# Performance work log

Hardware: AMD Instinct MI355X
Metric: run time of the kernel (lower is better)

## Reference

```python
import jax, jax.numpy as jnp
import numpy as np

DIM = 192
HEADS = 16
DIM_HEAD = 64
INNER = HEADS * DIM_HEAD  # 1024
B, N = 8, 1024


def setup_inputs() -> dict:
    key = jax.random.key(0)
    ks = jax.random.split(key, 8)
    x = jax.random.normal(ks[0], (B, N, DIM), dtype=jnp.float32)
    shift = jax.random.normal(ks[1], (B, 1, DIM), dtype=jnp.float32)
    scale = jax.random.normal(ks[2], (B, 1, DIM), dtype=jnp.float32)
    norm_w = jnp.ones((DIM,), dtype=jnp.float32)
    norm_b = jnp.zeros((DIM,), dtype=jnp.float32)
    w_qkv = jax.random.normal(ks[3], (DIM, 3 * INNER), dtype=jnp.float32) * (DIM ** -0.5)
    w_out = jax.random.normal(ks[4], (INNER, DIM), dtype=jnp.float32) * (INNER ** -0.5)
    b_out = jnp.zeros((DIM,), dtype=jnp.float32)
    return {"x": x, "shift": shift, "scale": scale, "norm_w": norm_w,
            "norm_b": norm_b, "w_qkv": w_qkv, "w_out": w_out, "b_out": b_out}


def _layernorm(x, w, b, eps=1e-5):
    mu = jnp.mean(x, axis=-1, keepdims=True)
    var = jnp.mean(jnp.square(x - mu), axis=-1, keepdims=True)
    return (x - mu) * jax.lax.rsqrt(var + eps) * w + b


def reference(x, shift, scale, norm_w, norm_b, w_qkv, w_out, b_out):
    h = _layernorm(x, norm_w, norm_b)
    h = h * (1.0 + scale) + shift  # adaLN modulation, broadcast over tokens
    qkv = h @ w_qkv  # [B, N, 3*INNER]
    q, k, v = jnp.split(qkv, 3, axis=-1)
    # [B, N, INNER] -> [B, H, N, Dh]
    def split_heads(t):
        return t.reshape(B, N, HEADS, DIM_HEAD).transpose(0, 2, 1, 3)
    q, k, v = split_heads(q), split_heads(k), split_heads(v)
    scores = jnp.einsum('bhnd,bhmd->bhnm', q, k) * (DIM_HEAD ** -0.5)
    attn = jax.nn.softmax(scores, axis=-1)
    out = jnp.einsum('bhnm,bhmd->bhnd', attn, v)  # [B, H, N, Dh]
    out = out.transpose(0, 2, 1, 3).reshape(B, N, INNER)
    return out @ w_out + b_out
```

## Files before the change

kernel.cpp:

```cpp
#include <hip/hip_runtime.h>

#define DIM 192
#define NB 8
#define NTOK 1024
#define HEADS 16
#define DH 64
#define INNER 1024
#define ROWS (NB * NTOK)

typedef __bf16 bf16x8 __attribute__((ext_vector_type(8)));
typedef float f32x4 __attribute__((ext_vector_type(4)));
typedef float f32x16 __attribute__((ext_vector_type(16)));
typedef unsigned int u32x4 __attribute__((ext_vector_type(4)));

__device__ inline unsigned short f2bf(float f) {
    union { float f; unsigned u; } v; v.f = f;
    unsigned r = v.u + 0x7FFF + ((v.u >> 16) & 1);
    return (unsigned short)(r >> 16);
}

__device__ inline unsigned pk2(float a, float b) {
    __bf16 x = (__bf16)a, y = (__bf16)b;
    unsigned short ux = __builtin_bit_cast(unsigned short, x);
    unsigned short uy = __builtin_bit_cast(unsigned short, y);
    return (unsigned)ux | ((unsigned)uy << 16);
}

__device__ inline void gl_lds16(const unsigned short* g, unsigned short* l) {
    __builtin_amdgcn_global_load_lds(
        (const __attribute__((address_space(1))) void*)g,
        (__attribute__((address_space(3))) void*)l, 16, 0, 0);
}

__device__ inline size_t fragIdx(int row, int k, int depth) {
    return ((size_t)(row >> 5) * ((size_t)depth * 4) +
            (size_t)(((k >> 4) * 2 + ((k >> 3) & 1)) * 32 + (row & 31))) * 8 + (k & 7);
}

__global__ __launch_bounds__(256) void k_pre(
    const float* __restrict__ x, const float* __restrict__ shift,
    const float* __restrict__ scale, const float* __restrict__ nw,
    const float* __restrict__ nb, const float* __restrict__ wqkv,
    const float* __restrict__ wout,
    unsigned short* __restrict__ hF, unsigned short* __restrict__ wF,
    unsigned short* __restrict__ woF) {
    int bid = blockIdx.x;
    if (bid < 2048) {
        int row = bid * 4 + (threadIdx.x >> 6);
        int lane = threadIdx.x & 63;
        const float* xr = x + row * DIM;
        float v0 = xr[lane], v1 = xr[lane + 64], v2 = xr[lane + 128];
        float s = v0 + v1 + v2;
        #pragma unroll
        for (int m = 1; m < 64; m <<= 1) s += __shfl_xor(s, m);
        float mean = s * (1.0f / DIM);
        float d0 = v0 - mean, d1 = v1 - mean, d2 = v2 - mean;
        float q = d0 * d0 + d1 * d1 + d2 * d2;
        #pragma unroll
        for (int m = 1; m < 64; m <<= 1) q += __shfl_xor(q, m);
        float rs = rsqrtf(q * (1.0f / DIM) + 1e-5f);
        int b = row >> 10;
        float vv[3] = {v0, v1, v2};
        #pragma unroll
        for (int i = 0; i < 3; i++) {
            int d = lane + 64 * i;
            float val = (vv[i] - mean) * rs * nw[d] + nb[d];
            val = val * (1.0f + scale[b * DIM + d]) + shift[b * DIM + d];
            hF[fragIdx(row, d, DIM)] = f2bf(val);
        }
    } else if (bid < 4352) {
        int idx = (bid - 2048) * 256 + threadIdx.x;
        int k = idx / 3072, c = idx % 3072;
        wF[fragIdx(c, k, DIM)] = f2bf(wqkv[idx]);
    } else {
        int idx = (bid - 4352) * 256 + threadIdx.x;
        int k = idx / 192, c = idx % 192;
        woF[fragIdx(c, k, INNER)] = f2bf(wout[idx]);
    }
}

__global__ __launch_bounds__(256, 3) void k_qkv(
    const unsigned short* __restrict__ hF, const unsigned short* __restrict__ wF,
    unsigned short* __restrict__ qm, unsigned short* __restrict__ km,
    unsigned short* __restrict__ vtm) {
    const float QSC = 0.125f * 1.4426950408889634f;
    int tid = threadIdx.x;
    int wave = tid >> 6, lane = tid & 63;
    int l31 = lane & 31, hi = lane >> 5;
    int c0 = blockIdx.x * 64 + (wave >> 1) * 32;
    int typ = c0 >> 10;
    int hd  = (c0 & 1023) >> 6;
    int coff = c0 & 32;

    const unsigned short* Ab = wF + (size_t)(c0 >> 5) * 768 * 8;
    bf16x8 af[12];
    #pragma unroll
    for (int kc = 0; kc < 12; kc++)
        af[kc] = *(const bf16x8*)(Ab + ((kc * 2 + hi) * 32 + l31) * 8);

    #pragma unroll
    for (int ns = 0; ns < 2; ns++) {
        int n0 = blockIdx.y * 128 + (wave & 1) * 64 + ns * 32;
        const unsigned short* Bb = hF + (size_t)(n0 >> 5) * 768 * 8;
        f32x16 acc;
        #pragma unroll
        for (int r = 0; r < 16; r++) acc[r] = 0.f;
        #pragma unroll
        for (int kc = 0; kc < 12; kc++) {
            bf16x8 bf = *(const bf16x8*)(Bb + ((kc * 2 + hi) * 32 + l31) * 8);
            acc = __builtin_amdgcn_mfma_f32_32x32x16_bf16(af[kc], bf, acc, 0, 0, 0);
        }
        int n = n0 + l31, bb = n >> 10, nm = n & 1023;
        if (typ < 2) {
            float sc = (typ == 0) ? QSC : 1.0f;
            unsigned short* base = (typ == 0 ? qm : km) +
                ((size_t)(bb * 16 + hd) * 1024 + nm) * 64;
            #pragma unroll
            for (int rg = 0; rg < 4; rg++) {
                uint2 val;
                val.x = pk2(acc[rg * 4 + 0] * sc, acc[rg * 4 + 1] * sc);
                val.y = pk2(acc[rg * 4 + 2] * sc, acc[rg * 4 + 3] * sc);
                *(uint2*)(base + coff + rg * 8 + hi * 4) = val;
            }
        } else {
            unsigned short* base = vtm + (size_t)(bb * 16 + hd) * 65536 + nm;
            #pragma unroll
            for (int r = 0; r < 16; r++) {
                int d = coff + (r & 3) + 8 * (r >> 2) + 4 * hi;
                base[(size_t)d * 1024] = f2bf(acc[r]);
            }
        }
    }
}

__global__ __launch_bounds__(512, 4) void k_attn(
    const unsigned short* __restrict__ qm, const unsigned short* __restrict__ km,
    const unsigned short* __restrict__ vtm, unsigned short* __restrict__ attnF) {
    __shared__ __align__(128) unsigned short Kb[2][4096];
    __shared__ __align__(128) unsigned short Vb[3][4096];

    int tid = threadIdx.x;
    int wave = tid >> 6, lane = tid & 63;
    int l31 = lane & 31, hi = lane >> 5;
    int bh = blockIdx.x, qt = blockIdx.y;
    int qbase = qt * 256 + wave * 32;
    const unsigned short* Q = qm + (size_t)bh * NTOK * DH;
    const unsigned short* K = km + (size_t)bh * NTOK * DH;
    const unsigned short* VT = vtm + (size_t)bh * DH * NTOK;

    bf16x8 qf[4];
    #pragma unroll
    for (int c = 0; c < 4; c++)
        qf[c] = *(const bf16x8*)(Q + (qbase + l31) * DH + c * 16 + hi * 8);

    float l_half = 0.f;
    f32x16 accO[2];
    #pragma unroll
    for (int dt = 0; dt < 2; dt++)
        #pragma unroll
        for (int r = 0; r < 16; r++) accO[dt][r] = 0.f;

    auto stageK = [&](int b, int t) {
        int off = tid * 16;
        int row = off >> 7, col = off & 127;
        int scol = col ^ ((row & 7) << 4);
        gl_lds16(K + (t * 64 + row) * DH + (scol >> 1),
                 (unsigned short*)((char*)Kb[b] + off));
    };
    auto stageV = [&](int b, int t) {
        int off = tid * 16;
        int row = off >> 7, col = off & 127;
        int scol = col ^ ((row & 7) << 4);
        gl_lds16(VT + (size_t)row * NTOK + t * 64 + (scol >> 1),
                 (unsigned short*)((char*)Vb[b] + off));
    };
    auto ldK = [&](int b, int row, int col) -> bf16x8 {
        int scol = col ^ ((row & 7) << 4);
        return *(const bf16x8*)((const char*)Kb[b] + row * 128 + scol);
    };
    auto ldV = [&](int b, int row, int col) -> bf16x8 {
        int scol = col ^ ((row & 7) << 4);
        return *(const bf16x8*)((const char*)Vb[b] + row * 128 + scol);
    };
    auto packP = [&](const f32x16& P, bf16x8& w0, bf16x8& w1) {
        u32x4 A, B;
        {
            auto r0 = __builtin_amdgcn_permlane32_swap(pk2(P[0], P[1]), pk2(P[4], P[5]), false, false);
            auto r1 = __builtin_amdgcn_permlane32_swap(pk2(P[2], P[3]), pk2(P[6], P[7]), false, false);
            A[0] = r0[0]; A[1] = r1[0]; A[2] = r0[1]; A[3] = r1[1];
        }
        {
            auto r0 = __builtin_amdgcn_permlane32_swap(pk2(P[8], P[9]), pk2(P[12], P[13]), false, false);
            auto r1 = __builtin_amdgcn_permlane32_swap(pk2(P[10], P[11]), pk2(P[14], P[15]), false, false);
            B[0] = r0[0]; B[1] = r1[0]; B[2] = r0[1]; B[3] = r1[1];
        }
        w0 = __builtin_bit_cast(bf16x8, A);
        w1 = __builtin_bit_cast(bf16x8, B);
    };

    bf16x8 pw[4];

    stageK(0, 0); stageV(0, 0);
    __syncthreads();

    stageK(1, 1); stageV(1, 1);
    {
        f32x16 C0, C1;
        #pragma unroll
        for (int r = 0; r < 16; r++) { C0[r] = 0.f; C1[r] = 0.f; }
        __builtin_amdgcn_s_setprio(1);
        #pragma unroll
        for (int c = 0; c < 4; c++) {
            bf16x8 kf = ldK(0, l31, c * 32 + hi * 16);
            C0 = __builtin_amdgcn_mfma_f32_32x32x16_bf16(kf, qf[c], C0, 0, 0, 0);
            bf16x8 kf2 = ldK(0, 32 + l31, c * 32 + hi * 16);
            C1 = __builtin_amdgcn_mfma_f32_32x32x16_bf16(kf2, qf[c], C1, 0, 0, 0);
        }
        __builtin_amdgcn_s_setprio(0);
        #pragma unroll
        for (int r = 0; r < 16; r++) {
            C0[r] = __builtin_amdgcn_exp2f(C0[r]);
            C1[r] = __builtin_amdgcn_exp2f(C1[r]);
        }
        float ps = 0.f;
        #pragma unroll
        for (int r = 0; r < 16; r++) ps += C0[r] + C1[r];
        l_half += ps;
        packP(C0, pw[0], pw[1]);
        packP(C1, pw[2], pw[3]);
        __syncthreads();
    }

    for (int t = 1; t < 16; t++) {
        int kc = t & 1;
        int vp = (t - 1) % 3;
        if (t < 15) { stageK((t + 1) & 1, t + 1); stageV((t + 1) % 3, t + 1); }

        f32x16 C0, C1;
        #pragma unroll
        for (int r = 0; r < 16; r++) { C0[r] = 0.f; C1[r] = 0.f; }
        __builtin_amdgcn_s_setprio(1);
        #pragma unroll
        for (int c = 0; c < 4; c++) {
            bf16x8 kf = ldK(kc, l31, c * 32 + hi * 16);
            C0 = __builtin_amdgcn_mfma_f32_32x32x16_bf16(kf, qf[c], C0, 0, 0, 0);
            bf16x8 kf2 = ldK(kc, 32 + l31, c * 32 + hi * 16);
            C1 = __builtin_amdgcn_mfma_f32_32x32x16_bf16(kf2, qf[c], C1, 0, 0, 0);
        }
        #pragma unroll
        for (int dt = 0; dt < 2; dt++) {
            #pragma unroll
            for (int kcc = 0; kcc < 4; kcc++) {
                bf16x8 vf = ldV(vp, dt * 32 + l31, kcc * 32 + hi * 16);
                accO[dt] = __builtin_amdgcn_mfma_f32_32x32x16_bf16(vf, pw[kcc], accO[dt], 0, 0, 0);
            }
        }
        __builtin_amdgcn_s_setprio(0);

        #pragma unroll
        for (int r = 0; r < 16; r++) {
            C0[r] = __builtin_amdgcn_exp2f(C0[r]);
            C1[r] = __builtin_amdgcn_exp2f(C1[r]);
        }
        float ps = 0.f;
        #pragma unroll
        for (int r = 0; r < 16; r++) ps += C0[r] + C1[r];
        l_half += ps;
        packP(C0, pw[0], pw[1]);
        packP(C1, pw[2], pw[3]);
        __syncthreads();
    }

    __builtin_amdgcn_s_setprio(1);
    #pragma unroll
    for (int dt = 0; dt < 2; dt++) {
        #pragma unroll
        for (int kcc = 0; kcc < 4; kcc++) {
            bf16x8 vf = ldV(0, dt * 32 + l31, kcc * 32 + hi * 16);
            accO[dt] = __builtin_amdgcn_mfma_f32_32x32x16_bf16(vf, pw[kcc], accO[dt], 0, 0, 0);
        }
    }
    __builtin_amdgcn_s_setprio(0);

    float l = l_half + __shfl_xor(l_half, 32);
    float inv = 1.0f / l;
    int b = bh >> 4, hd = bh & 15;
    int rowblk = b * 32 + qt * 8 + wave;
    #pragma unroll
    for (int dt = 0; dt < 2; dt++)
        #pragma unroll
        for (int rq = 0; rq < 4; rq++) {
            int g = (hd * 4 + dt * 2 + (rq >> 1)) * 2 + (rq & 1);
            uint2 val;
            val.x = pk2(accO[dt][rq * 4 + 0] * inv, accO[dt][rq * 4 + 1] * inv);
            val.y = pk2(accO[dt][rq * 4 + 2] * inv, accO[dt][rq * 4 + 3] * inv);
            *(uint2*)((char*)attnF + ((size_t)rowblk * 4096 + g * 32 + l31) * 16 + hi * 8) = val;
        }
}

__global__ __launch_bounds__(256, 2) void k_out(
    const unsigned short* __restrict__ attnF, const unsigned short* __restrict__ woF,
    const float* __restrict__ bias, float* __restrict__ out) {
    int wave = threadIdx.x >> 6, lane = threadIdx.x & 63;
    int l31 = lane & 31, hi = lane >> 5;
    int W = blockIdx.x * 4 + wave;
    int nb = W / 6, cb = W % 6;
    const unsigned short* A = attnF + (size_t)nb * 4096 * 8;
    const unsigned short* B = woF + (size_t)cb * 4096 * 8;

    f32x16 acc;
    #pragma unroll
    for (int r = 0; r < 16; r++) acc[r] = 0.f;
    #pragma unroll 16
    for (int kc = 0; kc < 64; kc++) {
        bf16x8 a = *(const bf16x8*)(A + ((kc * 2 + hi) * 32 + l31) * 8);
        bf16x8 b = *(const bf16x8*)(B + ((kc * 2 + hi) * 32 + l31) * 8);
        acc = __builtin_amdgcn_mfma_f32_32x32x16_bf16(a, b, acc, 0, 0, 0);
    }
    float bi = bias[cb * 32 + l31];
    #pragma unroll
    for (int r = 0; r < 16; r++) {
        int n = nb * 32 + (r & 3) + 8 * (r >> 2) + 4 * hi;
        out[(size_t)n * DIM + cb * 32 + l31] = acc[r] + bi;
    }
}

extern "C" void kernel_launch(void* const* d_in, const int* in_sizes, int n_in,
                              void* d_out, int out_size, void* d_ws, size_t ws_size,
                              hipStream_t stream) {
    const float* x     = (const float*)d_in[0];
    const float* shift = (const float*)d_in[1];
    const float* scale = (const float*)d_in[2];
    const float* nw    = (const float*)d_in[3];
    const float* nbv   = (const float*)d_in[4];
    const float* wqkv  = (const float*)d_in[5];
    const float* wout  = (const float*)d_in[6];
    const float* bout  = (const float*)d_in[7];
    float* out = (float*)d_out;

    char* ws = (char*)d_ws;
    unsigned short* hF    = (unsigned short*)(ws + 0);
    unsigned short* wF    = (unsigned short*)(ws + 3145728);
    unsigned short* woF   = (unsigned short*)(ws + 3145728 + 1179648);
    unsigned short* qm    = (unsigned short*)(ws + 4718592);
    unsigned short* km    = (unsigned short*)(ws + 4718592 + 16777216);
    unsigned short* vtm   = (unsigned short*)(ws + 4718592 + 2 * 16777216);
    unsigned short* attnF = (unsigned short*)(ws + 4718592 + 3 * 16777216);

    k_pre<<<dim3(5120), dim3(256), 0, stream>>>(x, shift, scale, nw, nbv, wqkv, wout, hF, wF, woF);
    k_qkv<<<dim3(48, 64), dim3(256), 0, stream>>>(hF, wF, qm, km, vtm);
    k_attn<<<dim3(128, 4), dim3(512), 0, stream>>>(qm, km, vtm, attnF);
    k_out<<<dim3(384), dim3(256), 0, stream>>>(attnF, woF, bout, out);
}
```

Measured before the change: 99.40 us.

## Triple-buffer K, use vmcnt-based waits, and compute softmax row sums via MFMA

Extends K staging to three LDS slots so K is prefetched two tiles ahead and V one ahead, replacing __syncthreads with explicit s_waitcnt vmcnt plus s_barrier. This is meant to cut load stalls at each iteration's barrier. The per-lane scalar row-sum reduction and cross-half shuffle are replaced by extra MFMAs against a ones vector, accumulated in accL. The final step adds and then subtracts the last P tile to cancel the duplicate accumulation. The cost is more LDS per block and extra MFMA work, and the sum now uses bf16-rounded P values.

```diff
diff --git a/kernel.cpp b/kernel.cpp
--- a/kernel.cpp
+++ b/kernel.cpp
@@ -136,7 +136,7 @@
 __global__ __launch_bounds__(512, 4) void k_attn(
     const unsigned short* __restrict__ qm, const unsigned short* __restrict__ km,
     const unsigned short* __restrict__ vtm, unsigned short* __restrict__ attnF) {
-    __shared__ __align__(128) unsigned short Kb[2][4096];
+    __shared__ __align__(128) unsigned short Kb[3][4096];
     __shared__ __align__(128) unsigned short Vb[3][4096];
 
     int tid = threadIdx.x;
@@ -153,34 +153,34 @@
     for (int c = 0; c < 4; c++)
         qf[c] = *(const bf16x8*)(Q + (qbase + l31) * DH + c * 16 + hi * 8);
 
-    float l_half = 0.f;
-    f32x16 accO[2];
-    #pragma unroll
-    for (int dt = 0; dt < 2; dt++)
-        #pragma unroll
-        for (int r = 0; r < 16; r++) accO[dt][r] = 0.f;
-
-    auto stageK = [&](int b, int t) {
+    u32x4 ov; ov[0] = 0x3F803F80u; ov[1] = 0x3F803F80u; ov[2] = 0x3F803F80u; ov[3] = 0x3F803F80u;
+    bf16x8 ones = __builtin_bit_cast(bf16x8, ov);
+
+    f32x16 accO[2], accL;
+    #pragma unroll
+    for (int r = 0; r < 16; r++) { accO[0][r] = 0.f; accO[1][r] = 0.f; accL[r] = 0.f; }
+
+    auto stageK = [&](int slot, int t) {
         int off = tid * 16;
         int row = off >> 7, col = off & 127;
         int scol = col ^ ((row & 7) << 4);
         gl_lds16(K + (t * 64 + row) * DH + (scol >> 1),
-                 (unsigned short*)((char*)Kb[b] + off));
-    };
-    auto stageV = [&](int b, int t) {
+                 (unsigned short*)((char*)Kb[slot] + off));
+    };
+    auto stageV = [&](int slot, int t) {
         int off = tid * 16;
         int row = off >> 7, col = off & 127;
         int scol = col ^ ((row & 7) << 4);
         gl_lds16(VT + (size_t)row * NTOK + t * 64 + (scol >> 1),
-                 (unsigned short*)((char*)Vb[b] + off));
-    };
-    auto ldK = [&](int b, int row, int col) -> bf16x8 {
+                 (unsigned short*)((char*)Vb[slot] + off));
+    };
+    auto ldK = [&](int slot, int row, int col) -> bf16x8 {
         int scol = col ^ ((row & 7) << 4);
-        return *(const bf16x8*)((const char*)Kb[b] + row * 128 + scol);
-    };
-    auto ldV = [&](int b, int row, int col) -> bf16x8 {
+        return *(const bf16x8*)((const char*)Kb[slot] + row * 128 + scol);
+    };
+    auto ldV = [&](int slot, int row, int col) -> bf16x8 {
         int scol = col ^ ((row & 7) << 4);
-        return *(const bf16x8*)((const char*)Vb[b] + row * 128 + scol);
+        return *(const bf16x8*)((const char*)Vb[slot] + row * 128 + scol);
     };
     auto packP = [&](const f32x16& P, bf16x8& w0, bf16x8& w1) {
         u32x4 A, B;
@@ -200,77 +200,63 @@
 
     bf16x8 pw[4];
 
-    stageK(0, 0); stageV(0, 0);
-    __syncthreads();
-
-    stageK(1, 1); stageV(1, 1);
-    {
+    stageK(0, 0);
+    stageV(0, 0);
+    stageK(1, 1);
+
+    #pragma unroll 1
+    for (int t = 0; t < 16; t++) {
+        if (t == 0 || t == 15) {
+            asm volatile("s_waitcnt vmcnt(1)" ::: "memory");
+        } else {
+            asm volatile("s_waitcnt vmcnt(2)" ::: "memory");
+        }
+        __builtin_amdgcn_s_barrier();
+        __builtin_amdgcn_sched_barrier(0);
+
+        if (t <= 13) stageK((t + 2) % 3, t + 2);
+        if (t <= 14) stageV((t + 1) % 3, t + 1);
+
+        int ks = t % 3;
         f32x16 C0, C1;
         #pragma unroll
         for (int r = 0; r < 16; r++) { C0[r] = 0.f; C1[r] = 0.f; }
         __builtin_amdgcn_s_setprio(1);
         #pragma unroll
         for (int c = 0; c < 4; c++) {
-            bf16x8 kf = ldK(0, l31, c * 32 + hi * 16);
+            bf16x8 kf = ldK(ks, l31, c * 32 + hi * 16);
             C0 = __builtin_amdgcn_mfma_f32_32x32x16_bf16(kf, qf[c], C0, 0, 0, 0);
-            bf16x8 kf2 = ldK(0, 32 + l31, c * 32 + hi * 16);
+            bf16x8 kf2 = ldK(ks, 32 + l31, c * 32 + hi * 16);
             C1 = __builtin_amdgcn_mfma_f32_32x32x16_bf16(kf2, qf[c], C1, 0, 0, 0);
         }
+        if (t >= 1) {
+            int vs = (t - 1) % 3;
+            #pragma unroll
+            for (int dt = 0; dt < 2; dt++) {
+                #pragma unroll
+                for (int kcc = 0; kcc < 4; kcc++) {
+                    bf16x8 vf = ldV(vs, dt * 32 + l31, kcc * 32 + hi * 16);
+                    accO[dt] = __builtin_amdgcn_mfma_f32_32x32x16_bf16(vf, pw[kcc], accO[dt], 0, 0, 0);
+                }
+            }
+        }
         __builtin_amdgcn_s_setprio(0);
+
         #pragma unroll
         for (int r = 0; r < 16; r++) {
             C0[r] = __builtin_amdgcn_exp2f(C0[r]);
             C1[r] = __builtin_amdgcn_exp2f(C1[r]);
         }
-        float ps = 0.f;
-        #pragma unroll
-        for (int r = 0; r < 16; r++) ps += C0[r] + C1[r];
-        l_half += ps;
         packP(C0, pw[0], pw[1]);
         packP(C1, pw[2], pw[3]);
-        __syncthreads();
-    }
-
-    for (int t = 1; t < 16; t++) {
-        int kc = t & 1;
-        int vp = (t - 1) % 3;
-        if (t < 15) { stageK((t + 1) & 1, t + 1); stageV((t + 1) % 3, t + 1); }
-
-        f32x16 C0, C1;
-        #pragma unroll
-        for (int r = 0; r < 16; r++) { C0[r] = 0.f; C1[r] = 0.f; }
-        __builtin_amdgcn_s_setprio(1);
-        #pragma unroll
-        for (int c = 0; c < 4; c++) {
-            bf16x8 kf = ldK(kc, l31, c * 32 + hi * 16);
-            C0 = __builtin_amdgcn_mfma_f32_32x32x16_bf16(kf, qf[c], C0, 0, 0, 0);
-            bf16x8 kf2 = ldK(kc, 32 + l31, c * 32 + hi * 16);
-            C1 = __builtin_amdgcn_mfma_f32_32x32x16_bf16(kf2, qf[c], C1, 0, 0, 0);
-        }
-        #pragma unroll
-        for (int dt = 0; dt < 2; dt++) {
-            #pragma unroll
-            for (int kcc = 0; kcc < 4; kcc++) {
-                bf16x8 vf = ldV(vp, dt * 32 + l31, kcc * 32 + hi * 16);
-                accO[dt] = __builtin_amdgcn_mfma_f32_32x32x16_bf16(vf, pw[kcc], accO[dt], 0, 0, 0);
-            }
-        }
-        __builtin_amdgcn_s_setprio(0);
-
-        #pragma unroll
-        for (int r = 0; r < 16; r++) {
-            C0[r] = __builtin_amdgcn_exp2f(C0[r]);
-            C1[r] = __builtin_amdgcn_exp2f(C1[r]);
-        }
-        float ps = 0.f;
-        #pragma unroll
-        for (int r = 0; r < 16; r++) ps += C0[r] + C1[r];
-        l_half += ps;
-        packP(C0, pw[0], pw[1]);
-        packP(C1, pw[2], pw[3]);
-        __syncthreads();
-    }
-
+        #pragma unroll
+        for (int kcc = 0; kcc < 4; kcc++)
+            accL = __builtin_amdgcn_mfma_f32_32x32x16_bf16(ones, pw[kcc], accL, 0, 0, 0);
+    }
+
+    asm volatile("s_waitcnt vmcnt(0)" ::: "memory");
+    __builtin_amdgcn_s_barrier();
+    __builtin_amdgcn_sched_barrier(0);
     __builtin_amdgcn_s_setprio(1);
     #pragma unroll
     for (int dt = 0; dt < 2; dt++) {
@@ -281,8 +267,17 @@
         }
     }
     __builtin_amdgcn_s_setprio(0);
-
-    float l = l_half + __shfl_xor(l_half, 32);
+    #pragma unroll
+    for (int kcc = 0; kcc < 4; kcc++)
+        accL = __builtin_amdgcn_mfma_f32_32x32x16_bf16(ones, pw[kcc], accL, 0, 0, 0);
+    #pragma unroll
+    for (int kcc = 0; kcc < 4; kcc++) {
+        u32x4 nv; nv[0] = 0xBF80BF80u; nv[1] = 0xBF80BF80u; nv[2] = 0xBF80BF80u; nv[3] = 0xBF80BF80u;
+        bf16x8 nones = __builtin_bit_cast(bf16x8, nv);
+        accL = __builtin_amdgcn_mfma_f32_32x32x16_bf16(nones, pw[kcc], accL, 0, 0, 0);
+    }
+
+    float l = accL[0];
     float inv = 1.0f / l;
     int b = bh >> 4, hd = bh & 15;
     int rowblk = b * 32 + qt * 8 + wave;
```

Result: slower. 105.4 us (+6.1%).
